# Optimization experiments

Hardware: AMD Instinct MI355X
Metric: run time of the kernel (lower is better)

The kernel has to match this reference:

```python
import jax, jax.numpy as jnp
import numpy as np

T, B, I, H = 512, 128, 256, 256
P = 0.25          # fixed dropout rate (float branch of p_logit)
EPS = 1e-07
TEMP = 0.1


def _concrete_mask(u, p):
    # (1 - sigmoid((log(p+eps)-log(1-p+eps)+log(u+eps)-log(1-u+eps))/t)) / (1-p)
    logit_p = jnp.log(p + EPS) - jnp.log(1.0 - p + EPS)
    logit_u = jnp.log(u + EPS) - jnp.log(1.0 - u + EPS)
    return (1.0 - jax.nn.sigmoid((logit_p + logit_u) / TEMP)) / (1.0 - p)


def setup_inputs() -> dict:
    key = jax.random.key(0)
    ks = jax.random.split(key, 7)
    k_scale = 1.0 / np.sqrt(H)  # matches uniform(-k, k) scale in init_weights
    inp = {
        "input": jax.random.normal(ks[0], (T, B, I), dtype=jnp.float32),
        "ux": jax.random.uniform(ks[1], (4, B, I), dtype=jnp.float32),
        "uh": jax.random.uniform(ks[2], (4, B, H), dtype=jnp.float32),
        "W": jax.random.normal(ks[3], (4, H, I), dtype=jnp.float32) * k_scale,
        "Wb": jax.random.normal(ks[4], (4, H), dtype=jnp.float32) * k_scale,
        "U": jax.random.normal(ks[5], (4, H, H), dtype=jnp.float32) * k_scale,
        "Ub": jax.random.normal(ks[6], (4, H), dtype=jnp.float32) * k_scale,
    }
    return inp


def reference(input, ux, uh, W, Wb, U, Ub):
    # Dropout masks (sampled once, shared across all timesteps), gate order i,f,o,g
    zx = _concrete_mask(ux, P)  # (4, B, I)
    zh = _concrete_mask(uh, P)  # (4, B, H)

    # Input-side gate pre-activations for ALL timesteps at once:
    # x_g[t] = (input[t] * zx[g]) @ W[g].T + Wb[g]  -> (T, B, 4, H)
    xm = input[:, None, :, :] * zx[None]                 # (T, 4, B, I)
    x_pre = jnp.einsum("tgbi,ghi->tbgh", xm, W) + Wb     # (T, B, 4, H)

    h0 = jnp.zeros((B, H), dtype=input.dtype)
    c0 = jnp.zeros((B, H), dtype=input.dtype)

    def step(carry, pre_t):
        h, c = carry
        hm = h[None] * zh                                 # (4, B, H)
        s = pre_t + jnp.einsum("gbh,gkh->bgk", hm, U) + Ub  # (B, 4, H)
        i = jax.nn.sigmoid(s[:, 0])
        f = jax.nn.sigmoid(s[:, 1])
        o = jax.nn.sigmoid(s[:, 2])
        g = jnp.tanh(s[:, 3])
        c = f * c + i * g
        h = o * jnp.tanh(c)
        return (h, c), h

    (h_t, c_t), hn = jax.lax.scan(step, (h0, c0), x_pre)
    return hn, h_t, c_t
```

## Files before the change

kernel.cpp:

```cpp
#include <hip/hip_runtime.h>
#include <hip/hip_bf16.h>

#define T_STEPS 512
#define B_SZ    128
#define I_SZ    256
#define H_SZ    256
#define NB      16
#define SCAN_BLOCKS (B_SZ / NB)
#define SCAN_THREADS 512

typedef __attribute__((ext_vector_type(8))) short short8;
typedef __attribute__((ext_vector_type(4))) float floatx4;
union I4S8 { uint4 u; short8 s; };

#define HM_G_STRIDE 8320
#define ST_OFF      33280
#define ST_ROW      268
#define ULDS_OFF    (ST_OFF + 64 * ST_ROW * 4)
#define ULDS_W      7168
#define SMEM_BYTES  (ULDS_OFF + 8 * ULDS_W)

static constexpr int SORD[8][8] = {
    {-1,-1,-1,-1,-1, 0, 2, 4},
    {-1,-1,-1,-1,-1, 1, 3, 5},
    {-1,-1,-1,-1,-1, 6, 8,10},
    {-1,-1,-1,-1,-1, 7, 9,11},
    {-1,-1,-1,-1,-1,12,14,16},
    {-1,-1,-1,-1,-1,13,15,17},
    {-1,-1,-1,-1,-1,19,21,23},
    {-1,-1,-1,-1,18,20,22,24},
};
static constexpr int SFRG[25] = {
     5,13, 6,14, 7,15,
    21,29,22,30,23,31,
    37,45,38,46,39,47,
    60,53,61,54,62,55,63
};

__device__ __forceinline__ float fast_sigmoid(float x) {
    return 1.f / (1.f + __expf(-x));
}
__device__ __forceinline__ float fast_tanh(float x) {
    float ax = fabsf(x);
    float e = __expf(-2.f * ax);
    float t = (1.f - e) / (1.f + e);
    return copysignf(t, x);
}
__device__ __forceinline__ ushort f2bf(float v) {
    __hip_bfloat16 hb = __float2bfloat16(v);
    return *(ushort*)&hb;
}
__device__ __forceinline__ float bf2f(ushort u) {
    unsigned int b = ((unsigned int)u) << 16;
    return __uint_as_float(b);
}
__device__ __forceinline__ float concrete_mask(float u) {
    const float EPS = 1e-7f;
    float logit_p = logf(0.25f + EPS) - logf(0.75f + EPS);
    float lu = logf(u + EPS) - logf(1.0f - u + EPS);
    float z = (logit_p + lu) * 10.0f;
    float sig = 1.0f / (1.0f + expf(-z));
    return (1.0f - sig) * (1.0f / 0.75f);
}

__global__ void mask_kernel(const float* __restrict__ ux, const float* __restrict__ uh,
                            float* __restrict__ zx, __hip_bfloat16* __restrict__ zh) {
    int idx = blockIdx.x * blockDim.x + threadIdx.x;
    const int n = 4 * B_SZ * I_SZ;
    if (idx < n) zx[idx] = concrete_mask(ux[idx]);
    else         zh[idx - n] = __float2bfloat16(concrete_mask(uh[idx - n]));
}

__global__ void uswz_kernel(const float* __restrict__ M, __hip_bfloat16* __restrict__ M_sw) {
    int tId = blockIdx.x * 256 + threadIdx.x;
    int lane  = tId & 63;
    int kk    = (tId >> 6) & 7;
    int ktile = (tId >> 9) & 15;
    int g     = tId >> 13;
    int nCol  = ktile * 16 + (lane & 15);
    int h0    = kk * 32 + ((lane >> 4) & 3) * 8;
    const float* src = M + ((size_t)g * 256 + nCol) * 256 + h0;
    ushort o[8];
    #pragma unroll
    for (int j = 0; j < 8; ++j) o[j] = f2bf(src[j]);
    uint4 pk;
    pk.x = (uint)o[0] | ((uint)o[1] << 16);
    pk.y = (uint)o[2] | ((uint)o[3] << 16);
    pk.z = (uint)o[4] | ((uint)o[5] << 16);
    pk.w = (uint)o[6] | ((uint)o[7] << 16);
    ((uint4*)M_sw)[tId] = pk;
}

__global__ __launch_bounds__(512, 2) void xpre_mfma_kernel(
        const float* __restrict__ input, const float* __restrict__ zx,
        const __hip_bfloat16* __restrict__ W_sw,
        const float* __restrict__ Wb, const float* __restrict__ Ub,
        __hip_bfloat16* __restrict__ xpre) {
    const int tid   = threadIdx.x;
    const int w     = tid >> 6;
    const int lane  = tid & 63;
    const int g     = w >> 1;
    const int khalf = w & 1;
    const int row0  = blockIdx.x * 64;
    const int mrow  = lane & 15;
    const int kq    = lane >> 4;

    floatx4 acc[4][8];
    #pragma unroll
    for (int mt = 0; mt < 4; ++mt)
        #pragma unroll
        for (int nt = 0; nt < 8; ++nt)
            #pragma unroll
            for (int r = 0; r < 4; ++r) acc[mt][nt][r] = 0.f;

    const uint4* Wp = (const uint4*)W_sw + ((size_t)((g * 16 + khalf * 8) * 8)) * 64 + lane;

    for (int kc = 0; kc < 8; ++kc) {
        I4S8 af[4];
        const int i0 = kc * 32 + kq * 8;
        #pragma unroll
        for (int mt = 0; mt < 4; ++mt) {
            int row = row0 + mt * 16 + mrow;
            int b   = row & (B_SZ - 1);
            const float4* ip = (const float4*)(input + (size_t)row * I_SZ + i0);
            const float4* zp = (const float4*)(zx + ((size_t)g * B_SZ + b) * I_SZ + i0);
            float4 a0 = ip[0], a1 = ip[1];
            float4 z0 = zp[0], z1 = zp[1];
            uint4 pk;
            pk.x = (uint)f2bf(a0.x * z0.x) | ((uint)f2bf(a0.y * z0.y) << 16);
            pk.y = (uint)f2bf(a0.z * z0.z) | ((uint)f2bf(a0.w * z0.w) << 16);
            pk.z = (uint)f2bf(a1.x * z1.x) | ((uint)f2bf(a1.y * z1.y) << 16);
            pk.w = (uint)f2bf(a1.z * z1.z) | ((uint)f2bf(a1.w * z1.w) << 16);
            af[mt].u = pk;
        }
        #pragma unroll
        for (int nt = 0; nt < 8; ++nt) {
            I4S8 bb; bb.u = Wp[(nt * 8 + kc) * 64];
            #pragma unroll
            for (int mt = 0; mt < 4; ++mt)
                acc[mt][nt] = __builtin_amdgcn_mfma_f32_16x16x32_bf16(af[mt].s, bb.s, acc[mt][nt], 0, 0, 0);
        }
    }
    #pragma unroll
    for (int nt = 0; nt < 8; ++nt) {
        int col = khalf * 128 + nt * 16 + (lane & 15);
        float bias = Wb[g * H_SZ + col] + Ub[g * H_SZ + col];
        #pragma unroll
        for (int mt = 0; mt < 4; ++mt) {
            #pragma unroll
            for (int r = 0; r < 4; ++r) {
                int row = row0 + mt * 16 + (lane >> 4) * 4 + r;
                xpre[((size_t)row * 4 + g) * H_SZ + col] = __float2bfloat16(acc[mt][nt][r] + bias);
            }
        }
    }
}

__global__ __launch_bounds__(SCAN_THREADS, 2) void scan_mfma_kernel(
        const __hip_bfloat16* __restrict__ xpre,
        const __hip_bfloat16* __restrict__ zh,
        const __hip_bfloat16* __restrict__ U_sw,
        float* __restrict__ out) {
    extern __shared__ __align__(16) char smem[];
    const int tid  = threadIdx.x;
    const int b0   = blockIdx.x * NB;
    const int w     = tid >> 6;
    const int lane  = tid & 63;
    const int g_w   = w >> 1;
    const int khalf = w & 1;
    const int be      = tid >> 5;
    const int k8      = (tid & 31) * 8;
    const int kk_e    = k8 >> 5;
    const int lane_hm = (be & 15) | (((k8 >> 3) & 3) << 4);

    const uint4* Uw = (const uint4*)U_sw + ((size_t)((g_w * 16 + khalf * 8) * 8)) * 64 + lane;
    float* st = (float*)(smem + ST_OFF);

    uint4 ures[32];
    #pragma unroll
    for (int nt = 0; nt < 8; ++nt)
        #pragma unroll
        for (int kk = 0; kk < 4; ++kk)
            ures[nt * 4 + kk] = Uw[(nt * 8 + kk) * 64];
    #pragma unroll
    for (int f = 0; f < 7; ++f) {
        uint4 v = Uw[(f * 8 + 4) * 64];
        *(uint4*)(smem + ULDS_OFF + w * ULDS_W + f * 1024 + lane * 16) = v;
    }
    for (int i = tid; i < HM_G_STRIDE * 4 / 16; i += SCAN_THREADS)
        ((uint4*)smem)[i] = make_uint4(0u, 0u, 0u, 0u);

    uint4 zhreg[4];
    float c8[8], h8[8];
    #pragma unroll
    for (int g = 0; g < 4; ++g)
        zhreg[g] = *(const uint4*)(zh + ((size_t)g * B_SZ + (b0 + be)) * H_SZ + k8);
    #pragma unroll
    for (int j = 0; j < 8; ++j) c8[j] = 0.f;

    __syncthreads();

    for (int t = 0; t < T_STEPS; ++t) {
        I4S8 afr[8];
        #pragma unroll
        for (int kk = 0; kk < 8; ++kk)
            afr[kk].u = *(const uint4*)(smem + g_w * HM_G_STRIDE + kk * 1040 + lane * 16);

        uint4 sbuf[4];
        #pragma unroll
        for (int q = 0; q < 4; ++q) sbuf[q] = Uw[SFRG[q] * 64];

        #pragma unroll
        for (int p = 0; p < 4; ++p) {
            floatx4 acc[2];
            #pragma unroll
            for (int e = 0; e < 2; ++e)
                #pragma unroll
                for (int r = 0; r < 4; ++r) acc[e][r] = 0.f;

            uint4 lb[2];
            #pragma unroll
            for (int e = 0; e < 2; ++e) {
                const int nt = 2 * p + e;
                if (nt < 7)
                    lb[e] = *(const uint4*)(smem + ULDS_OFF + w * ULDS_W + nt * 1024 + lane * 16);
            }

            #pragma unroll
            for (int kk = 0; kk < 8; ++kk) {
                #pragma unroll
                for (int e = 0; e < 2; ++e) {
                    const int nt = 2 * p + e;
                    I4S8 bb;
                    if (kk < 4) {
                        bb.u = ures[nt * 4 + kk];
                    } else if (kk == 4 && nt < 7) {
                        bb.u = lb[e];
                    } else {
                        const int o = SORD[nt][kk];
                        bb.u = sbuf[o & 3];
                        if (o + 4 < 25) sbuf[o & 3] = Uw[SFRG[o + 4] * 64];
                    }
                    acc[e] = __builtin_amdgcn_mfma_f32_16x16x32_bf16(afr[kk].s, bb.s, acc[e], 0, 0, 0);
                }
            }
            #pragma unroll
            for (int e = 0; e < 2; ++e) {
                const int nt = 2 * p + e;
                int kcol  = khalf * 128 + nt * 16 + (lane & 15);
                int brow4 = (lane >> 4) * 4;
                #pragma unroll
                for (int r = 0; r < 4; ++r)
                    st[((brow4 + r) * 4 + g_w) * ST_ROW + kcol] = acc[e][r];
            }
        }
        __syncthreads();

        uint4 xp[4];
        #pragma unroll
        for (int g = 0; g < 4; ++g)
            xp[g] = *(const uint4*)(xpre + (((size_t)t * B_SZ + (b0 + be)) * 4 + g) * H_SZ + k8);

        float sg[4][8];
        #pragma unroll
        for (int g = 0; g < 4; ++g) {
            const float* strow = st + ((be * 4 + g) * ST_ROW + k8);
            float4 lo = *(const float4*)(strow);
            float4 hi = *(const float4*)(strow + 4);
            sg[g][0] = lo.x; sg[g][1] = lo.y; sg[g][2] = lo.z; sg[g][3] = lo.w;
            sg[g][4] = hi.x; sg[g][5] = hi.y; sg[g][6] = hi.z; sg[g][7] = hi.w;
            const ushort* xs = (const ushort*)&xp[g];
            #pragma unroll
            for (int j = 0; j < 8; ++j) sg[g][j] += bf2f(xs[j]);
        }
        #pragma unroll
        for (int j = 0; j < 8; ++j) {
            float iv = fast_sigmoid(sg[0][j]);
            float fv = fast_sigmoid(sg[1][j]);
            float ov = fast_sigmoid(sg[2][j]);
            float gv = fast_tanh(sg[3][j]);
            float c  = fv * c8[j] + iv * gv;
            c8[j] = c;
            h8[j] = ov * fast_tanh(c);
        }
        {
            float* op = out + ((size_t)t * B_SZ + (b0 + be)) * H_SZ + k8;
            *(float4*)(op)     = make_float4(h8[0], h8[1], h8[2], h8[3]);
            *(float4*)(op + 4) = make_float4(h8[4], h8[5], h8[6], h8[7]);
        }
        #pragma unroll
        for (int g = 0; g < 4; ++g) {
            const ushort* zs = (const ushort*)&zhreg[g];
            uint4 pk;
            pk.x = (uint)f2bf(h8[0] * bf2f(zs[0])) | ((uint)f2bf(h8[1] * bf2f(zs[1])) << 16);
            pk.y = (uint)f2bf(h8[2] * bf2f(zs[2])) | ((uint)f2bf(h8[3] * bf2f(zs[3])) << 16);
            pk.z = (uint)f2bf(h8[4] * bf2f(zs[4])) | ((uint)f2bf(h8[5] * bf2f(zs[5])) << 16);
            pk.w = (uint)f2bf(h8[6] * bf2f(zs[6])) | ((uint)f2bf(h8[7] * bf2f(zs[7])) << 16);
            *(uint4*)(smem + g * HM_G_STRIDE + kk_e * 1040 + lane_hm * 16) = pk;
        }
        if (t == T_STEPS - 1) {
            size_t tail = (size_t)T_STEPS * B_SZ * H_SZ;
            float* hp = out + tail + (size_t)(b0 + be) * H_SZ + k8;
            float* cp = hp + (size_t)B_SZ * H_SZ;
            *(float4*)(hp)     = make_float4(h8[0], h8[1], h8[2], h8[3]);
            *(float4*)(hp + 4) = make_float4(h8[4], h8[5], h8[6], h8[7]);
            *(float4*)(cp)     = make_float4(c8[0], c8[1], c8[2], c8[3]);
            *(float4*)(cp + 4) = make_float4(c8[4], c8[5], c8[6], c8[7]);
        }
        __syncthreads();
    }
}

extern "C" void kernel_launch(void* const* d_in, const int* in_sizes, int n_in,
                              void* d_out, int out_size, void* d_ws, size_t ws_size,
                              hipStream_t stream) {
    const float* input = (const float*)d_in[0];
    const float* ux    = (const float*)d_in[1];
    const float* uh    = (const float*)d_in[2];
    const float* W     = (const float*)d_in[3];
    const float* Wb    = (const float*)d_in[4];
    const float* U     = (const float*)d_in[5];
    const float* Ub    = (const float*)d_in[6];
    float* out = (float*)d_out;

    float* zx            = (float*)d_ws;
    __hip_bfloat16* zh   = (__hip_bfloat16*)(zx + 4 * B_SZ * I_SZ);
    __hip_bfloat16* U_sw = zh + 4 * B_SZ * H_SZ;
    __hip_bfloat16* W_sw = U_sw + 4 * H_SZ * H_SZ;
    __hip_bfloat16* xpre = W_sw + 4 * H_SZ * I_SZ;

    mask_kernel<<<dim3(1024), dim3(256), 0, stream>>>(ux, uh, zx, zh);
    uswz_kernel<<<dim3(128), dim3(256), 0, stream>>>(U, U_sw);
    uswz_kernel<<<dim3(128), dim3(256), 0, stream>>>(W, W_sw);

    xpre_mfma_kernel<<<dim3(1024), dim3(512), 0, stream>>>(input, zx, W_sw, Wb, Ub, xpre);

    scan_mfma_kernel<<<dim3(SCAN_BLOCKS), dim3(SCAN_THREADS), SMEM_BYTES, stream>>>(
        xpre, zh, U_sw, out);
}
```

Measured before the change: 4.309 ms.

## Compute all four gates per wave and apply the LSTM cell directly from accumulators

The scan kernel now assigns each wave a 32-column slice of H across all four gates, so the gate pre-activations stay in MFMA accumulators. This removes the fp32 staging buffer in LDS and one of the two barriers per timestep. The masked hidden state is double-buffered in LDS, and the projection kernel writes xpre in a layout matching each scan thread for coalesced loads. In exchange, launch bounds fall to one block per SIMD, fewer weights are held in registers, and the hidden-state and output stores become scattered 2-byte and 4-byte writes.

```diff
diff --git a/kernel.cpp b/kernel.cpp
--- a/kernel.cpp
+++ b/kernel.cpp
@@ -13,28 +13,24 @@
 typedef __attribute__((ext_vector_type(4))) float floatx4;
 union I4S8 { uint4 u; short8 s; };
 
-#define HM_G_STRIDE 8320
-#define ST_OFF      33280
-#define ST_ROW      268
-#define ULDS_OFF    (ST_OFF + 64 * ST_ROW * 4)
-#define ULDS_W      7168
-#define SMEM_BYTES  (ULDS_OFF + 8 * ULDS_W)
-
-static constexpr int SORD[8][8] = {
-    {-1,-1,-1,-1,-1, 0, 2, 4},
-    {-1,-1,-1,-1,-1, 1, 3, 5},
-    {-1,-1,-1,-1,-1, 6, 8,10},
-    {-1,-1,-1,-1,-1, 7, 9,11},
-    {-1,-1,-1,-1,-1,12,14,16},
-    {-1,-1,-1,-1,-1,13,15,17},
-    {-1,-1,-1,-1,-1,19,21,23},
-    {-1,-1,-1,-1,18,20,22,24},
+#define HMB_STRIDE 33280
+#define ULDS_OFF   (2 * HMB_STRIDE)
+#define ULDS_W     7168
+#define SMEM_BYTES (ULDS_OFF + 8 * ULDS_W)
+
+static constexpr int SORD2[4][8][2] = {
+    { {-1,-1},{-1,-1},{-1,-1},{-1,-1},{-1,-1},{ 0, 1},{ 2, 3},{ 4, 5} },
+    { {-1,-1},{-1,-1},{-1,-1},{-1,-1},{-1,-1},{ 6, 7},{ 8, 9},{10,11} },
+    { {-1,-1},{-1,-1},{-1,-1},{-1,-1},{-1,-1},{12,13},{14,15},{16,17} },
+    { {18,19},{20,21},{22,23},{24,25},{-1,26},{27,28},{29,30},{31,32} },
 };
-static constexpr int SFRG[25] = {
-     5,13, 6,14, 7,15,
-    21,29,22,30,23,31,
-    37,45,38,46,39,47,
-    60,53,61,54,62,55,63
+static constexpr int OFS[33] = {
+      320,   832,   384,   896,   448,   960,
+     8512,  9024,  8576,  9088,  8640,  9152,
+    16704, 17216, 16768, 17280, 16832, 17344,
+    24576, 25088, 24640, 25152, 24704, 25216, 24768, 25280,
+    25344,
+    24896, 25408, 24960, 25472, 25024, 25536
 };
 
 __device__ __forceinline__ float fast_sigmoid(float x) {
@@ -143,169 +139,184 @@
     }
     #pragma unroll
     for (int nt = 0; nt < 8; ++nt) {
-        int col = khalf * 128 + nt * 16 + (lane & 15);
+        int col  = khalf * 128 + nt * 16 + (lane & 15);
         float bias = Wb[g * H_SZ + col] + Ub[g * H_SZ + col];
+        int np = col >> 5;
+        int e  = (col >> 4) & 1;
         #pragma unroll
         for (int mt = 0; mt < 4; ++mt) {
-            #pragma unroll
-            for (int r = 0; r < 4; ++r) {
-                int row = row0 + mt * 16 + (lane >> 4) * 4 + r;
-                xpre[((size_t)row * 4 + g) * H_SZ + col] = __float2bfloat16(acc[mt][nt][r] + bias);
-            }
+            int row = row0 + mt * 16 + (lane >> 4) * 4;
+            int t   = row >> 7;
+            int b   = row & (B_SZ - 1);
+            int blk = b >> 4;
+            int bi  = b & 15;
+            int tidp = np * 64 + (((bi >> 2) << 4) | (col & 15));
+            ushort q0 = f2bf(acc[mt][nt][0] + bias);
+            ushort q1 = f2bf(acc[mt][nt][1] + bias);
+            ushort q2 = f2bf(acc[mt][nt][2] + bias);
+            ushort q3 = f2bf(acc[mt][nt][3] + bias);
+            uint2 pk2;
+            pk2.x = (uint)q0 | ((uint)q1 << 16);
+            pk2.y = (uint)q2 | ((uint)q3 << 16);
+            size_t dst = ((((size_t)t * SCAN_BLOCKS + blk) * 512 + tidp) * 4 + g) * 8 + e * 4;
+            *(uint2*)(xpre + dst) = pk2;
         }
     }
 }
 
-__global__ __launch_bounds__(SCAN_THREADS, 2) void scan_mfma_kernel(
+__global__ __launch_bounds__(SCAN_THREADS, 1) void scan_mfma_kernel(
         const __hip_bfloat16* __restrict__ xpre,
         const __hip_bfloat16* __restrict__ zh,
         const __hip_bfloat16* __restrict__ U_sw,
         float* __restrict__ out) {
     extern __shared__ __align__(16) char smem[];
     const int tid  = threadIdx.x;
-    const int b0   = blockIdx.x * NB;
-    const int w     = tid >> 6;
-    const int lane  = tid & 63;
-    const int g_w   = w >> 1;
-    const int khalf = w & 1;
-    const int be      = tid >> 5;
-    const int k8      = (tid & 31) * 8;
-    const int kk_e    = k8 >> 5;
-    const int lane_hm = (be & 15) | (((k8 >> 3) & 3) << 4);
-
-    const uint4* Uw = (const uint4*)U_sw + ((size_t)((g_w * 16 + khalf * 8) * 8)) * 64 + lane;
-    float* st = (float*)(smem + ST_OFF);
-
-    uint4 ures[32];
-    #pragma unroll
-    for (int nt = 0; nt < 8; ++nt)
+    const int blk  = blockIdx.x;
+    const int b0   = blk * NB;
+    const int n    = tid >> 6;
+    const int lane = tid & 63;
+
+    const uint4* UB = (const uint4*)U_sw + n * 1024 + lane;
+
+    uint4 ures[24];
+    #pragma unroll
+    for (int g2 = 0; g2 < 6; ++g2)
         #pragma unroll
         for (int kk = 0; kk < 4; ++kk)
-            ures[nt * 4 + kk] = Uw[(nt * 8 + kk) * 64];
+            ures[g2 * 4 + kk] = UB[(g2 >> 1) * 8192 + (g2 & 1) * 512 + kk * 64];
     #pragma unroll
     for (int f = 0; f < 7; ++f) {
-        uint4 v = Uw[(f * 8 + 4) * 64];
-        *(uint4*)(smem + ULDS_OFF + w * ULDS_W + f * 1024 + lane * 16) = v;
+        uint4 v = UB[(f >> 1) * 8192 + (f & 1) * 512 + 4 * 64];
+        *(uint4*)(smem + ULDS_OFF + n * ULDS_W + f * 1024 + lane * 16) = v;
     }
-    for (int i = tid; i < HM_G_STRIDE * 4 / 16; i += SCAN_THREADS)
+    for (int i = tid; i < HMB_STRIDE / 16; i += SCAN_THREADS)
         ((uint4*)smem)[i] = make_uint4(0u, 0u, 0u, 0u);
 
-    uint4 zhreg[4];
+    uint zpk[4][4];
+    #pragma unroll
+    for (int g = 0; g < 4; ++g)
+        #pragma unroll
+        for (int e = 0; e < 2; ++e)
+            #pragma unroll
+            for (int rp = 0; rp < 2; ++rp) {
+                const __hip_bfloat16* zp = zh
+                    + ((size_t)(g * B_SZ + b0 + (lane >> 4) * 4 + rp * 2)) * H_SZ
+                    + n * 32 + e * 16 + (lane & 15);
+                ushort lo = *(const ushort*)zp;
+                ushort hi = *(const ushort*)(zp + H_SZ);
+                zpk[g][e * 2 + rp] = (uint)lo | ((uint)hi << 16);
+            }
+
     float c8[8], h8[8];
     #pragma unroll
-    for (int g = 0; g < 4; ++g)
-        zhreg[g] = *(const uint4*)(zh + ((size_t)g * B_SZ + (b0 + be)) * H_SZ + k8);
-    #pragma unroll
     for (int j = 0; j < 8; ++j) c8[j] = 0.f;
 
+    const int hm_lane_off = n * 1040 + (((lane & 15) >> 3) << 8)
+                          + ((lane >> 4) * 4) * 16 + (lane & 7) * 2;
+
     __syncthreads();
 
     for (int t = 0; t < T_STEPS; ++t) {
-        I4S8 afr[8];
-        #pragma unroll
-        for (int kk = 0; kk < 8; ++kk)
-            afr[kk].u = *(const uint4*)(smem + g_w * HM_G_STRIDE + kk * 1040 + lane * 16);
-
+        const char* hr = smem + (t & 1) * HMB_STRIDE + lane * 16;
+        char* hw = smem + ((t & 1) ^ 1) * HMB_STRIDE + hm_lane_off;
+
+        uint4 xpn[4];
+        #pragma unroll
+        for (int g = 0; g < 4; ++g)
+            xpn[g] = *(const uint4*)(xpre +
+                ((((size_t)t * SCAN_BLOCKS + blk) * 512 + tid) * 4 + g) * 8);
         uint4 sbuf[4];
         #pragma unroll
-        for (int q = 0; q < 4; ++q) sbuf[q] = Uw[SFRG[q] * 64];
-
-        #pragma unroll
-        for (int p = 0; p < 4; ++p) {
-            floatx4 acc[2];
-            #pragma unroll
-            for (int e = 0; e < 2; ++e)
-                #pragma unroll
-                for (int r = 0; r < 4; ++r) acc[e][r] = 0.f;
-
+        for (int q = 0; q < 4; ++q) sbuf[q] = UB[OFS[q]];
+
+        floatx4 acc[8];
+        #pragma unroll
+        for (int a = 0; a < 8; ++a)
+            #pragma unroll
+            for (int r = 0; r < 4; ++r) acc[a][r] = 0.f;
+
+        #pragma unroll
+        for (int g = 0; g < 4; ++g) {
+            I4S8 afr[8];
+            #pragma unroll
+            for (int kk = 0; kk < 8; ++kk)
+                afr[kk].u = *(const uint4*)(hr + g * 8320 + kk * 1040);
             uint4 lb[2];
-            #pragma unroll
-            for (int e = 0; e < 2; ++e) {
-                const int nt = 2 * p + e;
-                if (nt < 7)
-                    lb[e] = *(const uint4*)(smem + ULDS_OFF + w * ULDS_W + nt * 1024 + lane * 16);
-            }
+            lb[0] = *(const uint4*)(smem + ULDS_OFF + n * ULDS_W + (g * 2) * 1024 + lane * 16);
+            if (g < 3)
+                lb[1] = *(const uint4*)(smem + ULDS_OFF + n * ULDS_W + (g * 2 + 1) * 1024 + lane * 16);
 
             #pragma unroll
             for (int kk = 0; kk < 8; ++kk) {
                 #pragma unroll
                 for (int e = 0; e < 2; ++e) {
-                    const int nt = 2 * p + e;
                     I4S8 bb;
-                    if (kk < 4) {
-                        bb.u = ures[nt * 4 + kk];
-                    } else if (kk == 4 && nt < 7) {
+                    if (g < 3 && kk < 4) {
+                        bb.u = ures[(g * 2 + e) * 4 + kk];
+                    } else if (kk == 4 && !(g == 3 && e == 1)) {
                         bb.u = lb[e];
                     } else {
-                        const int o = SORD[nt][kk];
+                        const int o = SORD2[g][kk][e];
                         bb.u = sbuf[o & 3];
-                        if (o + 4 < 25) sbuf[o & 3] = Uw[SFRG[o + 4] * 64];
+                        if (o + 4 < 33) sbuf[o & 3] = UB[OFS[o + 4]];
                     }
-                    acc[e] = __builtin_amdgcn_mfma_f32_16x16x32_bf16(afr[kk].s, bb.s, acc[e], 0, 0, 0);
+                    acc[g * 2 + e] = __builtin_amdgcn_mfma_f32_16x16x32_bf16(
+                        afr[kk].s, bb.s, acc[g * 2 + e], 0, 0, 0);
                 }
             }
-            #pragma unroll
-            for (int e = 0; e < 2; ++e) {
-                const int nt = 2 * p + e;
-                int kcol  = khalf * 128 + nt * 16 + (lane & 15);
-                int brow4 = (lane >> 4) * 4;
+        }
+
+        float sg[4][8];
+        #pragma unroll
+        for (int g = 0; g < 4; ++g) {
+            const ushort* xs = (const ushort*)&xpn[g];
+            #pragma unroll
+            for (int i = 0; i < 8; ++i)
+                sg[g][i] = acc[g * 2 + (i >> 2)][i & 3] + bf2f(xs[i]);
+        }
+        #pragma unroll
+        for (int i = 0; i < 8; ++i) {
+            float iv = fast_sigmoid(sg[0][i]);
+            float fv = fast_sigmoid(sg[1][i]);
+            float ov = fast_sigmoid(sg[2][i]);
+            float gv = fast_tanh(sg[3][i]);
+            float c  = fv * c8[i] + iv * gv;
+            c8[i] = c;
+            h8[i] = ov * fast_tanh(c);
+        }
+        {
+            float* ob = out + ((size_t)t * B_SZ + b0 + (lane >> 4) * 4) * H_SZ
+                      + n * 32 + (lane & 15);
+            #pragma unroll
+            for (int e = 0; e < 2; ++e)
                 #pragma unroll
                 for (int r = 0; r < 4; ++r)
-                    st[((brow4 + r) * 4 + g_w) * ST_ROW + kcol] = acc[e][r];
-            }
-        }
-        __syncthreads();
-
-        uint4 xp[4];
+                    ob[(size_t)r * H_SZ + e * 16] = h8[e * 4 + r];
+        }
         #pragma unroll
         for (int g = 0; g < 4; ++g)
-            xp[g] = *(const uint4*)(xpre + (((size_t)t * B_SZ + (b0 + be)) * 4 + g) * H_SZ + k8);
-
-        float sg[4][8];
-        #pragma unroll
-        for (int g = 0; g < 4; ++g) {
-            const float* strow = st + ((be * 4 + g) * ST_ROW + k8);
-            float4 lo = *(const float4*)(strow);
-            float4 hi = *(const float4*)(strow + 4);
-            sg[g][0] = lo.x; sg[g][1] = lo.y; sg[g][2] = lo.z; sg[g][3] = lo.w;
-            sg[g][4] = hi.x; sg[g][5] = hi.y; sg[g][6] = hi.z; sg[g][7] = hi.w;
-            const ushort* xs = (const ushort*)&xp[g];
-            #pragma unroll
-            for (int j = 0; j < 8; ++j) sg[g][j] += bf2f(xs[j]);
-        }
-        #pragma unroll
-        for (int j = 0; j < 8; ++j) {
-            float iv = fast_sigmoid(sg[0][j]);
-            float fv = fast_sigmoid(sg[1][j]);
-            float ov = fast_sigmoid(sg[2][j]);
-            float gv = fast_tanh(sg[3][j]);
-            float c  = fv * c8[j] + iv * gv;
-            c8[j] = c;
-            h8[j] = ov * fast_tanh(c);
-        }
-        {
-            float* op = out + ((size_t)t * B_SZ + (b0 + be)) * H_SZ + k8;
-            *(float4*)(op)     = make_float4(h8[0], h8[1], h8[2], h8[3]);
-            *(float4*)(op + 4) = make_float4(h8[4], h8[5], h8[6], h8[7]);
-        }
-        #pragma unroll
-        for (int g = 0; g < 4; ++g) {
-            const ushort* zs = (const ushort*)&zhreg[g];
-            uint4 pk;
-            pk.x = (uint)f2bf(h8[0] * bf2f(zs[0])) | ((uint)f2bf(h8[1] * bf2f(zs[1])) << 16);
-            pk.y = (uint)f2bf(h8[2] * bf2f(zs[2])) | ((uint)f2bf(h8[3] * bf2f(zs[3])) << 16);
-            pk.z = (uint)f2bf(h8[4] * bf2f(zs[4])) | ((uint)f2bf(h8[5] * bf2f(zs[5])) << 16);
-            pk.w = (uint)f2bf(h8[6] * bf2f(zs[6])) | ((uint)f2bf(h8[7] * bf2f(zs[7])) << 16);
-            *(uint4*)(smem + g * HM_G_STRIDE + kk_e * 1040 + lane_hm * 16) = pk;
-        }
+            #pragma unroll
+            for (int e = 0; e < 2; ++e)
+                #pragma unroll
+                for (int r = 0; r < 4; ++r) {
+                    const int i = e * 4 + r;
+                    ushort zv = (ushort)(zpk[g][i >> 1] >> ((i & 1) * 16));
+                    ushort hv = f2bf(h8[i] * bf2f(zv));
+                    *(ushort*)(hw + g * 8320 + e * 512 + r * 16) = hv;
+                }
+
         if (t == T_STEPS - 1) {
             size_t tail = (size_t)T_STEPS * B_SZ * H_SZ;
-            float* hp = out + tail + (size_t)(b0 + be) * H_SZ + k8;
+            float* hp = out + tail + (size_t)(b0 + (lane >> 4) * 4) * H_SZ
+                      + n * 32 + (lane & 15);
             float* cp = hp + (size_t)B_SZ * H_SZ;
-            *(float4*)(hp)     = make_float4(h8[0], h8[1], h8[2], h8[3]);
-            *(float4*)(hp + 4) = make_float4(h8[4], h8[5], h8[6], h8[7]);
-            *(float4*)(cp)     = make_float4(c8[0], c8[1], c8[2], c8[3]);
-            *(float4*)(cp + 4) = make_float4(c8[4], c8[5], c8[6], c8[7]);
+            #pragma unroll
+            for (int e = 0; e < 2; ++e)
+                #pragma unroll
+                for (int r = 0; r < 4; ++r) {
+                    hp[(size_t)r * H_SZ + e * 16] = h8[e * 4 + r];
+                    cp[(size_t)r * H_SZ + e * 16] = c8[e * 4 + r];
+                }
         }
         __syncthreads();
     }
```

New measurement: 4.499 ms. 1.04x slower.
